# Kernel tuning notes

Hardware: AMD Instinct MI355X
Metric: run time of the kernel (lower is better)

## Reference

```python
import jax, jax.numpy as jnp
import numpy as np

B, S, E, H = 2, 2048, 1024, 16
HD = E // H  # head dim = 64
BASE = 10000.0


def _rope(x):
    # x: [b, h, s, hd]; interleaved RoPE (pairs (2i, 2i+1) rotated)
    s, hd = x.shape[-2], x.shape[-1]
    theta = 1.0 / (BASE ** (jnp.arange(0, hd, 2, dtype=jnp.float32) / hd))  # [hd/2]
    enc = jnp.arange(s, dtype=jnp.float32)[:, None] * theta[None, :]        # [s, hd/2]
    enc = jnp.repeat(enc, 2, axis=-1)                                        # [s, hd] interleaved
    cos, sin = jnp.cos(enc), jnp.sin(enc)
    # rotate_half: (x1, x2) -> (-x2, x1) on interleaved pairs
    xp = x.reshape(*x.shape[:-1], hd // 2, 2)
    rot = jnp.stack((-xp[..., 1], xp[..., 0]), axis=-1).reshape(x.shape)
    return x * cos + rot * sin


def reference(x, w1, w2):
    b, s, e = x.shape
    qkv = jnp.einsum('bse,fe->bsf', x, w1)                 # [b, s, 3e]
    qkv = qkv.reshape(b, s, 3, H, HD)                      # 'b s (n h e)'
    q, k, v = (jnp.transpose(qkv[:, :, i], (0, 2, 1, 3)) for i in range(3))  # [b,h,s,hd]
    q, k = _rope(q), _rope(k)
    scale = 1.0 / jnp.sqrt(jnp.asarray(HD, dtype=x.dtype))
    scores = jnp.einsum('bhqd,bhkd->bhqk', q, k) * scale   # [b,h,s,s]
    attn = jax.nn.softmax(scores, axis=-1)
    o = jnp.einsum('bhqk,bhkd->bhqd', attn, v)             # [b,h,s,hd]
    o = jnp.transpose(o, (0, 2, 1, 3)).reshape(b, s, e)    # 'b h s e -> b s (h e)'
    return jnp.einsum('bse,fe->bsf', o, w2)


def setup_inputs() -> dict:
    key = jax.random.key(0)
    k1, k2, k3 = jax.random.split(key, 3)
    x = jax.random.normal(k1, (B, S, E), dtype=jnp.float32)
    w1 = jax.random.normal(k2, (3 * E, E), dtype=jnp.float32) * (E ** -0.5)
    w2 = jax.random.normal(k3, (E, E), dtype=jnp.float32) * (E ** -0.5)
    return {"x": x, "w1": w1, "w2": w2}
```

## Files before the change

kernel.cpp:

```cpp
#include <hip/hip_runtime.h>
#include <math.h>

typedef unsigned short u16;
typedef unsigned int u32;
typedef float f32x4 __attribute__((ext_vector_type(4)));
typedef float f32x16 __attribute__((ext_vector_type(16)));
typedef u32 u32x4 __attribute__((ext_vector_type(4)));

static const size_t TAB_B  = 0;
static const size_t QBF_B  = 524288;
static const size_t KBF_B  = 8912896;
static const size_t VTB_B  = 17301504;
static const size_t W2H_B  = 25690112;
static const size_t XBF_B  = 29884416;
static const size_t W1BF_B = 38273024;
static const size_t O16_B  = 29884416;

#if __has_builtin(__builtin_amdgcn_exp2f)
#define EXP2(x) __builtin_amdgcn_exp2f(x)
#else
#define EXP2(x) __expf(0.69314718056f * (x))
#endif

__device__ __forceinline__ u16 f2bf(float f) {
  u32 u = __builtin_bit_cast(u32, f);
  u += 0x7fffu + ((u >> 16) & 1u);
  return (u16)(u >> 16);
}
__device__ __forceinline__ float bf2f(u16 h) {
  return __builtin_bit_cast(float, (u32)h << 16);
}
__device__ __forceinline__ u16 f2h(float f) {
  _Float16 h = (_Float16)f;
  return __builtin_bit_cast(u16, h);
}
__device__ __forceinline__ u32 cvtpk(float a, float b) {
  u32 r;
  asm("v_cvt_pk_bf16_f32 %0, %1, %2" : "=v"(r) : "v"(a), "v"(b));
  return r;
}
__device__ __forceinline__ void plswap(u32& a, u32& b) {
  asm volatile("v_permlane32_swap_b32 %0, %1" : "+v"(a), "+v"(b));
}
__device__ __forceinline__ void mfma16(f32x4& d, u32x4 a, u32x4 b) {
  asm volatile("v_mfma_f32_16x16x32_bf16 %0, %1, %2, %0"
               : "+v"(d)
               : "v"(a), "v"(b));
}
__device__ __forceinline__ void mfma16f(f32x4& d, u32x4 a, u32x4 b) {
  asm volatile("v_mfma_f32_16x16x32_f16 %0, %1, %2, %0"
               : "+v"(d)
               : "v"(a), "v"(b));
}
__device__ __forceinline__ void mfma32(f32x16& d, u32x4 a, u32x4 b) {
  asm volatile("v_mfma_f32_32x32x16_bf16 %0, %1, %2, %0"
               : "+v"(d)
               : "v"(a), "v"(b));
}
__device__ __forceinline__ void gld16(const void* g, void* l) {
  __builtin_amdgcn_global_load_lds(
      (const __attribute__((address_space(1))) void*)(void*)g,
      (__attribute__((address_space(3))) void*)l, 16, 0, 0);
}
#define HZ()                                            \
  do {                                                  \
    asm volatile("s_nop 7\ns_nop 7\ns_nop 7\ns_nop 7"); \
    __builtin_amdgcn_sched_barrier(0);                  \
  } while (0)
#define BAR()                          \
  do {                                 \
    __builtin_amdgcn_s_barrier();      \
    __builtin_amdgcn_sched_barrier(0); \
  } while (0)

__global__ __launch_bounds__(256) void prep_kernel(
    const float* __restrict__ x, const float* __restrict__ w1,
    const float* __restrict__ w2, float2* __restrict__ tab,
    u16* __restrict__ xbf, u16* __restrict__ w1bf, u16* __restrict__ w2h) {
  const int blk = blockIdx.x;
  const int t = threadIdx.x;
  if (blk < 256) {
    const int idx = (blk << 8) + t;
    const int s = idx >> 5, i = idx & 31;
    double theta = pow(10000.0, -((double)(2 * i)) / 64.0);
    float ang = (float)s * (float)theta;
    tab[idx] = make_float2(cosf(ang), sinf(ang));
  } else if (blk < 1280) {
    int i = ((blk - 256) << 8) + t;
#pragma unroll
    for (int r = 0; r < 4; ++r, i += 262144) {
      float4 v = ((const float4*)x)[i];
      ushort4 o;
      o.x = f2bf(v.x); o.y = f2bf(v.y); o.z = f2bf(v.z); o.w = f2bf(v.w);
      ((ushort4*)xbf)[i] = o;
    }
  } else if (blk < 2048) {
    int i = ((blk - 1280) << 8) + t;
#pragma unroll
    for (int r = 0; r < 4; ++r, i += 196608) {
      float4 v = ((const float4*)w1)[i];
      ushort4 o;
      o.x = f2bf(v.x); o.y = f2bf(v.y); o.z = f2bf(v.z); o.w = f2bf(v.w);
      ((ushort4*)w1bf)[i] = o;
    }
  } else {
    int i = ((blk - 2048) << 8) + t;
#pragma unroll
    for (int r = 0; r < 4; ++r, i += 65536) {
      float4 v = ((const float4*)w2)[i];
      ushort4 o;
      o.x = f2h(v.x); o.y = f2h(v.y); o.z = f2h(v.z); o.w = f2h(v.w);
      ((ushort4*)w2h)[i] = o;
    }
  }
}

template <int MODE, int NI>
__global__ __launch_bounds__(256) void gemm_bt(
    const u16* __restrict__ Ahi, const u16* __restrict__ Bhi, int nbn, int nkb,
    int cpx, const float2* __restrict__ tab, u16* __restrict__ qd,
    u16* __restrict__ kd, u16* __restrict__ vtd, float* __restrict__ fout) {
  __shared__ __align__(16) char SMEM[MODE == 0 ? 34816 : 16384 + NI * 4096];
  char* As = SMEM;
  char* Bs = SMEM + 16384;
  const int bid = blockIdx.x;
  const int wgid = (bid & 7) * cpx + (bid >> 3);
  const int bm = wgid / nbn;
  const int bn = wgid % nbn;
  const int m0 = bm << 7;
  const int n0 = bn * (NI << 5);
  const int t = threadIdx.x;
  const int w = t >> 6;
  const int lane = t & 63;
  const int lr = lane & 15;
  const int lg = lane >> 4;
  const int wr0 = (w >> 1) << 6;
  const int wc0 = (w & 1) * (NI << 4);
  const int srow0 = t >> 3;
  const int sblk = t & 7;

  f32x4 acc[4][NI];
#pragma unroll
  for (int mi = 0; mi < 4; ++mi)
#pragma unroll
    for (int ni = 0; ni < NI; ++ni) acc[mi][ni] = (f32x4)0.0f;

  for (int kb = 0; kb < nkb; ++kb) {
    const int k0 = kb << 6;
    if (kb) __syncthreads();
#pragma unroll
    for (int r = 0; r < 4; ++r) {
      const int row = srow0 + (r << 5);
      const int g = sblk ^ (row & 7);
      gld16(Ahi + (size_t)(m0 + row) * 1024 + k0 + (g << 3),
            As + (r << 12) + (w << 10));
    }
#pragma unroll
    for (int r = 0; r < NI; ++r) {
      const int row = srow0 + (r << 5);
      const int g = sblk ^ (row & 7);
      gld16(Bhi + (size_t)(n0 + row) * 1024 + k0 + (g << 3),
            Bs + (r << 12) + (w << 10));
    }
    asm volatile("s_waitcnt vmcnt(0)" ::: "memory");
    __syncthreads();
#pragma unroll
    for (int kk = 0; kk < 2; ++kk) {
      u32x4 af[4], bf[NI];
#pragma unroll
      for (int mi = 0; mi < 4; ++mi) {
        const int row = wr0 + (mi << 4) + lr;
        af[mi] = *(const u32x4*)(As + row * 128 +
                                 ((((kk << 2) + lg) ^ (row & 7)) << 4));
      }
#pragma unroll
      for (int ni = 0; ni < NI; ++ni) {
        const int row = wc0 + (ni << 4) + lr;
        bf[ni] = *(const u32x4*)(Bs + row * 128 +
                                 ((((kk << 2) + lg) ^ (row & 7)) << 4));
      }
      asm volatile("s_nop 1");
      __builtin_amdgcn_s_setprio(1);
#pragma unroll
      for (int mi = 0; mi < 4; ++mi)
#pragma unroll
        for (int ni = 0; ni < NI; ++ni) {
          if constexpr (MODE == 1)
            mfma16f(acc[mi][ni], af[mi], bf[ni]);
          else
            mfma16(acc[mi][ni], af[mi], bf[ni]);
        }
      __builtin_amdgcn_s_setprio(0);
    }
  }
  HZ();
  if constexpr (MODE == 0) {
    if (n0 >= 2048) {
      u16* Vt = (u16*)SMEM;
      __syncthreads();
#pragma unroll
      for (int mi = 0; mi < 4; ++mi)
#pragma unroll
        for (int ni = 0; ni < NI; ++ni)
#pragma unroll
          for (int i = 0; i < 4; ++i) {
            const int dl = wc0 + (ni << 4) + lr;
            const int sl = wr0 + (mi << 4) + (lg << 2) + i;
            Vt[dl * 136 + sl] = f2bf(acc[mi][ni][i]);
          }
      __syncthreads();
      const int row = t >> 1;
      const int half = t & 1;
      const int hh2 = (n0 - 2048 + row) >> 6;
      const int d2 = (n0 - 2048 + row) & 63;
      const int b2 = m0 >> 11;
      u16* dst = vtd + (((size_t)(b2 * 16 + hh2) * 64 + d2) * 2048) +
                 (m0 & 2047) + half * 64;
      const u16* src = Vt + row * 136 + half * 64;
#pragma unroll
      for (int c = 0; c < 8; ++c)
        *(u32x4*)(dst + (c << 3)) = *(const u32x4*)(src + (c << 3));
      return;
    }
  }
#pragma unroll
  for (int mi = 0; mi < 4; ++mi)
#pragma unroll
    for (int ni = 0; ni < NI; ++ni)
#pragma unroll
      for (int i = 0; i < 4; ++i) {
        float val = acc[mi][ni][i];
        const int grow = m0 + wr0 + (mi << 4) + (lg << 2) + i;
        const int col = n0 + wc0 + (ni << 4) + lr;
        if (MODE == 0) {
          const int b = grow >> 11, s = grow & 2047;
          const int which = col >> 10, hh = (col >> 6) & 15, d = col & 63;
          const size_t base = (size_t)((b << 4) + hh);
          float other = __shfl_xor(val, 1);
          float2 cs = tab[(s << 5) + (d >> 1)];
          float r = (d & 1) ? fmaf(val, cs.x, other * cs.y)
                            : fmaf(val, cs.x, -other * cs.y);
          if (which == 0) r *= 0.18033688011f;
          u16* dstp = which ? kd : qd;
          dstp[(base * 2048 + s) * 64 + d] = f2bf(r);
        } else {
          fout[(size_t)grow * 1024 + col] = val;
        }
      }
}

__global__ __launch_bounds__(256) void attn_mfma(
    const u16* __restrict__ q, const u16* __restrict__ k,
    const u16* __restrict__ vt, u16* __restrict__ o16) {
  __shared__ __align__(16) char Ks[2][8192];
  __shared__ __align__(16) char Vs[2][8192];
  const int bid = blockIdx.x;
  const int swz = (bid & 7) * 64 + (bid >> 3);
  const int qt = swz & 15;
  const int hh = (swz >> 4) & 15;
  const int b = swz >> 8;
  const int t = threadIdx.x;
  const int w = t >> 6;
  const int lane = t & 63;
  const int lq = lane & 31;
  const int h = lane >> 5;

  const size_t bh = (size_t)((b << 4) + hh);
  const u16* qb = q + (bh * 2048 + (size_t)(qt * 128 + w * 32)) * 64;
  const u16* kb = k + bh * 2048 * 64;
  const u16* vb = vt + bh * 64 * 2048;

  u32x4 qf[4];
#pragma unroll
  for (int dk = 0; dk < 4; ++dk)
    qf[dk] = *(const u32x4*)(qb + lq * 64 + dk * 16 + h * 8);

  auto issue = [&](int kt_, int buf_) {
    const u16* ksrc = kb + kt_ * 4096;
#pragma unroll
    for (int r = 0; r < 2; ++r) {
      const int row = (t >> 3) + (r << 5);
      const int g = (t & 7) ^ (row & 7);
      gld16(ksrc + row * 64 + (g << 3), &Ks[buf_][(r << 12) + (w << 10)]);
      gld16(vb + (size_t)row * 2048 + kt_ * 64 + (g << 3),
            &Vs[buf_][(r << 12) + (w << 10)]);
    }
  };

  f32x16 oacc0 = (f32x16)0.0f, oacc1 = (f32x16)0.0f;
  float lrow = 0.0f;

  issue(0, 0);
  for (int kt = 0; kt < 32; ++kt) {
    const int cur = kt & 1;
    if (kt < 31) {
      issue(kt + 1, cur ^ 1);
      asm volatile("s_waitcnt vmcnt(4)" ::: "memory");
    } else {
      asm volatile("s_waitcnt vmcnt(0)" ::: "memory");
    }
    BAR();
    const char* Kc = Ks[cur];
    const char* Vc = Vs[cur];
    f32x16 s0 = (f32x16)0.0f, s1 = (f32x16)0.0f;
    __builtin_amdgcn_s_setprio(1);
#pragma unroll
    for (int dk = 0; dk < 4; ++dk) {
      const int c = (dk << 1) + h;
      u32x4 kf0 = *(const u32x4*)(Kc + lq * 128 + ((c ^ (lq & 7)) << 4));
      u32x4 kf1 = *(const u32x4*)(Kc + (32 + lq) * 128 + ((c ^ (lq & 7)) << 4));
      mfma32(s0, kf0, qf[dk]);
      mfma32(s1, kf1, qf[dk]);
    }
    __builtin_amdgcn_s_setprio(0);
    HZ();
    float lsum = 0.0f;
#pragma unroll
    for (int i = 0; i < 16; ++i) {
      s0[i] = EXP2(s0[i]);
      lsum += s0[i];
    }
#pragma unroll
    for (int i = 0; i < 16; ++i) {
      s1[i] = EXP2(s1[i]);
      lsum += s1[i];
    }
    lrow += lsum;
    u32x4 pa0, pa1, pa2, pa3;
    {
      u32 w0 = cvtpk(s0[0], s0[1]), w1 = cvtpk(s0[2], s0[3]);
      u32 w2 = cvtpk(s0[4], s0[5]), w3 = cvtpk(s0[6], s0[7]);
      u32 w4 = cvtpk(s0[8], s0[9]), w5 = cvtpk(s0[10], s0[11]);
      u32 w6 = cvtpk(s0[12], s0[13]), w7 = cvtpk(s0[14], s0[15]);
      plswap(w0, w2);
      plswap(w1, w3);
      plswap(w4, w6);
      plswap(w5, w7);
      pa0[0] = w0; pa0[1] = w1; pa0[2] = w2; pa0[3] = w3;
      pa1[0] = w4; pa1[1] = w5; pa1[2] = w6; pa1[3] = w7;
      u32 y0 = cvtpk(s1[0], s1[1]), y1 = cvtpk(s1[2], s1[3]);
      u32 y2 = cvtpk(s1[4], s1[5]), y3 = cvtpk(s1[6], s1[7]);
      u32 y4 = cvtpk(s1[8], s1[9]), y5 = cvtpk(s1[10], s1[11]);
      u32 y6 = cvtpk(s1[12], s1[13]), y7 = cvtpk(s1[14], s1[15]);
      plswap(y0, y2);
      plswap(y1, y3);
      plswap(y4, y6);
      plswap(y5, y7);
      pa2[0] = y0; pa2[1] = y1; pa2[2] = y2; pa2[3] = y3;
      pa3[0] = y4; pa3[1] = y5; pa3[2] = y6; pa3[3] = y7;
    }
    asm volatile("s_nop 2");
    __builtin_amdgcn_s_setprio(1);
#define PVSTEP(kbk, paf)                                                      \
  {                                                                           \
    const int c = ((kbk) << 1) + h;                                           \
    u32x4 vf0 = *(const u32x4*)(Vc + lq * 128 + ((c ^ (lq & 7)) << 4));       \
    u32x4 vf1 =                                                               \
        *(const u32x4*)(Vc + (32 + lq) * 128 + ((c ^ (lq & 7)) << 4));        \
    mfma32(oacc0, paf, vf0);                                                  \
    mfma32(oacc1, paf, vf1);                                                  \
  }
    PVSTEP(0, pa0)
    PVSTEP(1, pa1)
    PVSTEP(2, pa2)
    PVSTEP(3, pa3)
#undef PVSTEP
    __builtin_amdgcn_s_setprio(0);
    BAR();
  }
  HZ();
  const float invl = 1.0f / (lrow + __shfl_xor(lrow, 32));
#pragma unroll
  for (int r = 0; r < 16; ++r) {
    const int qr = (r & 3) + 8 * (r >> 2) + 4 * h;
    const float fr = __shfl(invl, qr);
    const size_t srow = (size_t)(b * 2048 + (qt << 7) + (w << 5) + qr);
    const size_t base = srow * 1024 + (hh << 6) + lq;
    o16[base] = f2h(oacc0[r] * fr);
    o16[base + 32] = f2h(oacc1[r] * fr);
  }
}

extern "C" void kernel_launch(void* const* d_in, const int* in_sizes, int n_in,
                              void* d_out, int out_size, void* d_ws,
                              size_t ws_size, hipStream_t stream) {
  const float* x = (const float*)d_in[0];
  const float* w1 = (const float*)d_in[1];
  const float* w2 = (const float*)d_in[2];
  char* ws = (char*)d_ws;
  float2* tab = (float2*)(ws + TAB_B);
  u16* qbf = (u16*)(ws + QBF_B);
  u16* kbf = (u16*)(ws + KBF_B);
  u16* vtbf = (u16*)(ws + VTB_B);
  u16* w2h = (u16*)(ws + W2H_B);
  u16* xbf = (u16*)(ws + XBF_B);
  u16* w1bf = (u16*)(ws + W1BF_B);
  u16* o16 = (u16*)(ws + O16_B);
  float* out = (float*)d_out;

  prep_kernel<<<dim3(2304), dim3(256), 0, stream>>>(x, w1, w2, tab, xbf, w1bf,
                                                    w2h);
  gemm_bt<0, 4><<<dim3(32 * 24), dim3(256), 0, stream>>>(
      xbf, w1bf, 24, 16, 96, tab, qbf, kbf, vtbf, nullptr);
  attn_mfma<<<dim3(512), dim3(256), 0, stream>>>(qbf, kbf, vtbf, o16);
  gemm_bt<1, 2><<<dim3(32 * 16), dim3(256), 0, stream>>>(
      o16, w2h, 16, 16, 64, nullptr, nullptr, nullptr, nullptr, out);
}
```

Measured before the change: 106.1 us.

## Software-pipeline attention loop with triple-buffered LDS and overlapped QK/softmax-PV

Moves the K/V LDS staging from double to triple buffering and restructures the key-tile loop so the QK^T MFMAs for the next tile are issued alongside the exp/convert/PV work for the previous tile. The loop is manually unrolled by two with rotating score registers and buffer pointers, plus a prologue and epilogue. The aim is to hide softmax VALU latency behind matrix work and keep prefetches two tiles ahead. In exchange it uses more LDS (48KB per block), which can reduce occupancy, and holds more live registers for the two score sets.

```diff
diff --git a/kernel.cpp b/kernel.cpp
--- a/kernel.cpp
+++ b/kernel.cpp
@@ -252,8 +252,8 @@
 __global__ __launch_bounds__(256) void attn_mfma(
     const u16* __restrict__ q, const u16* __restrict__ k,
     const u16* __restrict__ vt, u16* __restrict__ o16) {
-  __shared__ __align__(16) char Ks[2][8192];
-  __shared__ __align__(16) char Vs[2][8192];
+  __shared__ __align__(16) char Ks0[8192], Ks1[8192], Ks2[8192];
+  __shared__ __align__(16) char Vs0[8192], Vs1[8192], Vs2[8192];
   const int bid = blockIdx.x;
   const int swz = (bid & 7) * 64 + (bid >> 3);
   const int qt = swz & 15;
@@ -275,99 +275,138 @@
   for (int dk = 0; dk < 4; ++dk)
     qf[dk] = *(const u32x4*)(qb + lq * 64 + dk * 16 + h * 8);
 
-  auto issue = [&](int kt_, int buf_) {
+  auto issue = [&](int kt_, char* kb_, char* vb_) {
     const u16* ksrc = kb + kt_ * 4096;
 #pragma unroll
     for (int r = 0; r < 2; ++r) {
       const int row = (t >> 3) + (r << 5);
       const int g = (t & 7) ^ (row & 7);
-      gld16(ksrc + row * 64 + (g << 3), &Ks[buf_][(r << 12) + (w << 10)]);
+      gld16(ksrc + row * 64 + (g << 3), kb_ + (r << 12) + (w << 10));
       gld16(vb + (size_t)row * 2048 + kt_ * 64 + (g << 3),
-            &Vs[buf_][(r << 12) + (w << 10)]);
+            vb_ + (r << 12) + (w << 10));
     }
   };
 
   f32x16 oacc0 = (f32x16)0.0f, oacc1 = (f32x16)0.0f;
   float lrow = 0.0f;
-
-  issue(0, 0);
-  for (int kt = 0; kt < 32; ++kt) {
-    const int cur = kt & 1;
-    if (kt < 31) {
-      issue(kt + 1, cur ^ 1);
-      asm volatile("s_waitcnt vmcnt(4)" ::: "memory");
-    } else {
-      asm volatile("s_waitcnt vmcnt(0)" ::: "memory");
-    }
-    BAR();
-    const char* Kc = Ks[cur];
-    const char* Vc = Vs[cur];
-    f32x16 s0 = (f32x16)0.0f, s1 = (f32x16)0.0f;
-    __builtin_amdgcn_s_setprio(1);
-#pragma unroll
-    for (int dk = 0; dk < 4; ++dk) {
-      const int c = (dk << 1) + h;
-      u32x4 kf0 = *(const u32x4*)(Kc + lq * 128 + ((c ^ (lq & 7)) << 4));
-      u32x4 kf1 = *(const u32x4*)(Kc + (32 + lq) * 128 + ((c ^ (lq & 7)) << 4));
-      mfma32(s0, kf0, qf[dk]);
-      mfma32(s1, kf1, qf[dk]);
-    }
-    __builtin_amdgcn_s_setprio(0);
-    HZ();
-    float lsum = 0.0f;
-#pragma unroll
-    for (int i = 0; i < 16; ++i) {
-      s0[i] = EXP2(s0[i]);
-      lsum += s0[i];
-    }
-#pragma unroll
-    for (int i = 0; i < 16; ++i) {
-      s1[i] = EXP2(s1[i]);
-      lsum += s1[i];
-    }
-    lrow += lsum;
-    u32x4 pa0, pa1, pa2, pa3;
-    {
-      u32 w0 = cvtpk(s0[0], s0[1]), w1 = cvtpk(s0[2], s0[3]);
-      u32 w2 = cvtpk(s0[4], s0[5]), w3 = cvtpk(s0[6], s0[7]);
-      u32 w4 = cvtpk(s0[8], s0[9]), w5 = cvtpk(s0[10], s0[11]);
-      u32 w6 = cvtpk(s0[12], s0[13]), w7 = cvtpk(s0[14], s0[15]);
-      plswap(w0, w2);
-      plswap(w1, w3);
-      plswap(w4, w6);
-      plswap(w5, w7);
-      pa0[0] = w0; pa0[1] = w1; pa0[2] = w2; pa0[3] = w3;
-      pa1[0] = w4; pa1[1] = w5; pa1[2] = w6; pa1[3] = w7;
-      u32 y0 = cvtpk(s1[0], s1[1]), y1 = cvtpk(s1[2], s1[3]);
-      u32 y2 = cvtpk(s1[4], s1[5]), y3 = cvtpk(s1[6], s1[7]);
-      u32 y4 = cvtpk(s1[8], s1[9]), y5 = cvtpk(s1[10], s1[11]);
-      u32 y6 = cvtpk(s1[12], s1[13]), y7 = cvtpk(s1[14], s1[15]);
-      plswap(y0, y2);
-      plswap(y1, y3);
-      plswap(y4, y6);
-      plswap(y5, y7);
-      pa2[0] = y0; pa2[1] = y1; pa2[2] = y2; pa2[3] = y3;
-      pa3[0] = y4; pa3[1] = y5; pa3[2] = y6; pa3[3] = y7;
-    }
-    asm volatile("s_nop 2");
-    __builtin_amdgcn_s_setprio(1);
-#define PVSTEP(kbk, paf)                                                      \
+  f32x16 sa0, sa1, sb0, sb1;
+  char *kA = Ks0, *kB = Ks1, *kC = Ks2;
+  char *vA = Vs0, *vB = Vs1, *vC = Vs2;
+
+#define QKSTEP(S0, S1, KCUR)                                                   \
   {                                                                           \
-    const int c = ((kbk) << 1) + h;                                           \
-    u32x4 vf0 = *(const u32x4*)(Vc + lq * 128 + ((c ^ (lq & 7)) << 4));       \
-    u32x4 vf1 =                                                               \
-        *(const u32x4*)(Vc + (32 + lq) * 128 + ((c ^ (lq & 7)) << 4));        \
-    mfma32(oacc0, paf, vf0);                                                  \
-    mfma32(oacc1, paf, vf1);                                                  \
-  }
-    PVSTEP(0, pa0)
-    PVSTEP(1, pa1)
-    PVSTEP(2, pa2)
-    PVSTEP(3, pa3)
-#undef PVSTEP
-    __builtin_amdgcn_s_setprio(0);
-    BAR();
-  }
+    S0 = (f32x16)0.0f;                                                        \
+    S1 = (f32x16)0.0f;                                                        \
+    __builtin_amdgcn_s_setprio(1);                                            \
+    _Pragma("unroll") for (int dk = 0; dk < 4; ++dk) {                        \
+      const int c = (dk << 1) + h;                                            \
+      u32x4 kf0 = *(const u32x4*)((KCUR) + lq * 128 + ((c ^ (lq & 7)) << 4)); \
+      u32x4 kf1 =                                                             \
+          *(const u32x4*)((KCUR) + (32 + lq) * 128 + ((c ^ (lq & 7)) << 4));  \
+      mfma32(S0, kf0, qf[dk]);                                                \
+      mfma32(S1, kf1, qf[dk]);                                                \
+    }                                                                         \
+    __builtin_amdgcn_s_setprio(0);                                            \
+  }
+
+#define SMPV(S0, S1, VCUR)                                                    \
+  {                                                                           \
+    float lsum = 0.0f;                                                        \
+    _Pragma("unroll") for (int i = 0; i < 16; ++i) {                          \
+      S0[i] = EXP2(S0[i]);                                                    \
+      lsum += S0[i];                                                          \
+    }                                                                         \
+    _Pragma("unroll") for (int i = 0; i < 16; ++i) {                          \
+      S1[i] = EXP2(S1[i]);                                                    \
+      lsum += S1[i];                                                          \
+    }                                                                         \
+    lrow += lsum;                                                             \
+    u32x4 pa0, pa1, pa2, pa3;                                                 \
+    {                                                                         \
+      u32 w0 = cvtpk(S0[0], S0[1]), w1 = cvtpk(S0[2], S0[3]);                 \
+      u32 w2 = cvtpk(S0[4], S0[5]), w3 = cvtpk(S0[6], S0[7]);                 \
+      u32 w4 = cvtpk(S0[8], S0[9]), w5 = cvtpk(S0[10], S0[11]);               \
+      u32 w6 = cvtpk(S0[12], S0[13]), w7 = cvtpk(S0[14], S0[15]);             \
+      plswap(w0, w2);                                                         \
+      plswap(w1, w3);                                                         \
+      plswap(w4, w6);                                                         \
+      plswap(w5, w7);                                                         \
+      pa0[0] = w0; pa0[1] = w1; pa0[2] = w2; pa0[3] = w3;                     \
+      pa1[0] = w4; pa1[1] = w5; pa1[2] = w6; pa1[3] = w7;                     \
+      u32 y0 = cvtpk(S1[0], S1[1]), y1 = cvtpk(S1[2], S1[3]);                 \
+      u32 y2 = cvtpk(S1[4], S1[5]), y3 = cvtpk(S1[6], S1[7]);                 \
+      u32 y4 = cvtpk(S1[8], S1[9]), y5 = cvtpk(S1[10], S1[11]);               \
+      u32 y6 = cvtpk(S1[12], S1[13]), y7 = cvtpk(S1[14], S1[15]);             \
+      plswap(y0, y2);                                                         \
+      plswap(y1, y3);                                                         \
+      plswap(y4, y6);                                                         \
+      plswap(y5, y7);                                                         \
+      pa2[0] = y0; pa2[1] = y1; pa2[2] = y2; pa2[3] = y3;                     \
+      pa3[0] = y4; pa3[1] = y5; pa3[2] = y6; pa3[3] = y7;                     \
+    }                                                                         \
+    asm volatile("s_nop 2");                   \
+    __builtin_amdgcn_s_setprio(1);                                            \
+    {                                                                         \
+      u32x4 vf0, vf1;                                                         \
+      vf0 = *(const u32x4*)((VCUR) + lq * 128 + (((0 + h) ^ (lq & 7)) << 4)); \
+      vf1 = *(const u32x4*)((VCUR) + (32 + lq) * 128 +                        \
+                            (((0 + h) ^ (lq & 7)) << 4));                     \
+      mfma32(oacc0, pa0, vf0);                                                \
+      mfma32(oacc1, pa0, vf1);                                                \
+      vf0 = *(const u32x4*)((VCUR) + lq * 128 + (((2 + h) ^ (lq & 7)) << 4)); \
+      vf1 = *(const u32x4*)((VCUR) + (32 + lq) * 128 +                        \
+                            (((2 + h) ^ (lq & 7)) << 4));                     \
+      mfma32(oacc0, pa1, vf0);                                                \
+      mfma32(oacc1, pa1, vf1);                                                \
+      vf0 = *(const u32x4*)((VCUR) + lq * 128 + (((4 + h) ^ (lq & 7)) << 4)); \
+      vf1 = *(const u32x4*)((VCUR) + (32 + lq) * 128 +                        \
+                            (((4 + h) ^ (lq & 7)) << 4));                     \
+      mfma32(oacc0, pa2, vf0);                                                \
+      mfma32(oacc1, pa2, vf1);                                                \
+      vf0 = *(const u32x4*)((VCUR) + lq * 128 + (((6 + h) ^ (lq & 7)) << 4)); \
+      vf1 = *(const u32x4*)((VCUR) + (32 + lq) * 128 +                        \
+                            (((6 + h) ^ (lq & 7)) << 4));                     \
+      mfma32(oacc0, pa3, vf0);                                                \
+      mfma32(oacc1, pa3, vf1);                                                \
+    }                                                                         \
+    __builtin_amdgcn_s_setprio(0);                                            \
+  }
+
+#define BODY(KT, SP0, SP1, SN0, SN1)                                          \
+  {                                                                           \
+    if ((KT) + 2 < 32) {                                                      \
+      issue((KT) + 2, kC, vC);                                                \
+      asm volatile("s_waitcnt vmcnt(4)" ::: "memory");                        \
+    } else {                                                                  \
+      asm volatile("s_waitcnt vmcnt(0)" ::: "memory");                        \
+    }                                                                         \
+    BAR();                                                                    \
+    QKSTEP(SN0, SN1, kB)                                                      \
+    SMPV(SP0, SP1, vA)                                                        \
+    BAR();                                                                    \
+    {                                                                         \
+      char* tk = kA; kA = kB; kB = kC; kC = tk;                               \
+      char* tv = vA; vA = vB; vB = vC; vC = tv;                               \
+    }                                                                         \
+  }
+
+  issue(0, kA, vA);
+  issue(1, kB, vB);
+  asm volatile("s_waitcnt vmcnt(4)" ::: "memory");
+  BAR();
+  QKSTEP(sa0, sa1, kA)
+  HZ();
+  for (int p = 0; p < 15; ++p) {
+    const int kt = p << 1;
+    BODY(kt, sa0, sa1, sb0, sb1)
+    BODY(kt + 1, sb0, sb1, sa0, sa1)
+  }
+  BODY(30, sa0, sa1, sb0, sb1)
+  HZ();
+  SMPV(sb0, sb1, vA)
+#undef BODY
+#undef SMPV
+#undef QKSTEP
   HZ();
   const float invl = 1.0f / (lrow + __shfl_xor(lrow, 32));
 #pragma unroll
```

Result: no change. 105.5 us (-0.6%).

## Double attention KV tile to 128 keys per iteration with wider V swizzle

Applied to the files above, without the earlier changes.

The attention loop now stages 128 keys per iteration instead of 64, which halves the iteration count and the number of barriers. K and V LDS buffers double in size, and the V tile is laid out with 16-chunk rows and a matching XOR swizzle. Each iteration computes four score tiles and runs exp/pack/PV in two halves, and the row-sum exp accumulation now uses a tree reduction. The cost is more LDS (64KB per block) and more registers, which may lower occupancy.

```diff
diff --git a/kernel.cpp b/kernel.cpp
--- a/kernel.cpp
+++ b/kernel.cpp
@@ -252,8 +252,8 @@
 __global__ __launch_bounds__(256) void attn_mfma(
     const u16* __restrict__ q, const u16* __restrict__ k,
     const u16* __restrict__ vt, u16* __restrict__ o16) {
-  __shared__ __align__(16) char Ks[2][8192];
-  __shared__ __align__(16) char Vs[2][8192];
+  __shared__ __align__(16) char Ks[2][16384];
+  __shared__ __align__(16) char Vs[2][16384];
   const int bid = blockIdx.x;
   const int swz = (bid & 7) * 64 + (bid >> 3);
   const int qt = swz & 15;
@@ -276,26 +276,85 @@
     qf[dk] = *(const u32x4*)(qb + lq * 64 + dk * 16 + h * 8);
 
   auto issue = [&](int kt_, int buf_) {
-    const u16* ksrc = kb + kt_ * 4096;
-#pragma unroll
-    for (int r = 0; r < 2; ++r) {
-      const int row = (t >> 3) + (r << 5);
-      const int g = (t & 7) ^ (row & 7);
-      gld16(ksrc + row * 64 + (g << 3), &Ks[buf_][(r << 12) + (w << 10)]);
-      gld16(vb + (size_t)row * 2048 + kt_ * 64 + (g << 3),
-            &Vs[buf_][(r << 12) + (w << 10)]);
+    const u16* ksrc = kb + (size_t)kt_ * 8192;
+#pragma unroll
+    for (int r = 0; r < 4; ++r) {
+      const int ci = (r << 8) + (w << 6) + lane;
+      const int dstb = ((r << 8) + (w << 6)) << 4;
+      {
+        const int row = ci >> 3, ch = ci & 7;
+        const int g = ch ^ (row & 7);
+        gld16(ksrc + row * 64 + (g << 3), &Ks[buf_][dstb]);
+      }
+      {
+        const int row = ci >> 4, ch = ci & 15;
+        const int g = ch ^ (row & 15);
+        gld16(vb + (size_t)row * 2048 + kt_ * 128 + (g << 3), &Vs[buf_][dstb]);
+      }
     }
   };
 
   f32x16 oacc0 = (f32x16)0.0f, oacc1 = (f32x16)0.0f;
   float lrow = 0.0f;
 
+#define EXPTREE(S)                                                            \
+  {                                                                           \
+    _Pragma("unroll") for (int i = 0; i < 16; ++i) S[i] = EXP2(S[i]);         \
+    float a0 = (S[0] + S[1]) + (S[2] + S[3]);                                 \
+    float a1 = (S[4] + S[5]) + (S[6] + S[7]);                                 \
+    float a2 = (S[8] + S[9]) + (S[10] + S[11]);                               \
+    float a3 = (S[12] + S[13]) + (S[14] + S[15]);                             \
+    lrow += (a0 + a1) + (a2 + a3);                                            \
+  }
+
+#define PACK(S0, S1)                                                          \
+  {                                                                           \
+    u32 w0 = cvtpk(S0[0], S0[1]), w1 = cvtpk(S0[2], S0[3]);                   \
+    u32 w2 = cvtpk(S0[4], S0[5]), w3 = cvtpk(S0[6], S0[7]);                   \
+    u32 w4 = cvtpk(S0[8], S0[9]), w5 = cvtpk(S0[10], S0[11]);                 \
+    u32 w6 = cvtpk(S0[12], S0[13]), w7 = cvtpk(S0[14], S0[15]);               \
+    plswap(w0, w2);                                                           \
+    plswap(w1, w3);                                                           \
+    plswap(w4, w6);                                                           \
+    plswap(w5, w7);                                                           \
+    pa0[0] = w0; pa0[1] = w1; pa0[2] = w2; pa0[3] = w3;                       \
+    pa1[0] = w4; pa1[1] = w5; pa1[2] = w6; pa1[3] = w7;                       \
+    u32 y0 = cvtpk(S1[0], S1[1]), y1 = cvtpk(S1[2], S1[3]);                   \
+    u32 y2 = cvtpk(S1[4], S1[5]), y3 = cvtpk(S1[6], S1[7]);                   \
+    u32 y4 = cvtpk(S1[8], S1[9]), y5 = cvtpk(S1[10], S1[11]);                 \
+    u32 y6 = cvtpk(S1[12], S1[13]), y7 = cvtpk(S1[14], S1[15]);               \
+    plswap(y0, y2);                                                           \
+    plswap(y1, y3);                                                           \
+    plswap(y4, y6);                                                           \
+    plswap(y5, y7);                                                           \
+    pa2[0] = y0; pa2[1] = y1; pa2[2] = y2; pa2[3] = y3;                       \
+    pa3[0] = y4; pa3[1] = y5; pa3[2] = y6; pa3[3] = y7;                       \
+  }
+
+#define PVH(VCUR, JB)                                                         \
+  asm volatile("s_nop 2");                                                    \
+  __builtin_amdgcn_s_setprio(1);                                              \
+  {                                                                           \
+    u32x4 vf0, vf1;                                                           \
+    _Pragma("unroll") for (int kbk = 0; kbk < 4; ++kbk) {                     \
+      const int jc = (JB) + (kbk << 1) + h;                                   \
+      const int co = (jc ^ (lq & 15)) << 4;                                   \
+      vf0 = *(const u32x4*)((VCUR) + lq * 256 + co);                          \
+      vf1 = *(const u32x4*)((VCUR) + (32 + lq) * 256 + co);                   \
+      if (kbk == 0) { mfma32(oacc0, pa0, vf0); mfma32(oacc1, pa0, vf1); }     \
+      if (kbk == 1) { mfma32(oacc0, pa1, vf0); mfma32(oacc1, pa1, vf1); }     \
+      if (kbk == 2) { mfma32(oacc0, pa2, vf0); mfma32(oacc1, pa2, vf1); }     \
+      if (kbk == 3) { mfma32(oacc0, pa3, vf0); mfma32(oacc1, pa3, vf1); }     \
+    }                                                                         \
+  }                                                                           \
+  __builtin_amdgcn_s_setprio(0);
+
   issue(0, 0);
-  for (int kt = 0; kt < 32; ++kt) {
+  for (int kt = 0; kt < 16; ++kt) {
     const int cur = kt & 1;
-    if (kt < 31) {
+    if (kt < 15) {
       issue(kt + 1, cur ^ 1);
-      asm volatile("s_waitcnt vmcnt(4)" ::: "memory");
+      asm volatile("s_waitcnt vmcnt(8)" ::: "memory");
     } else {
       asm volatile("s_waitcnt vmcnt(0)" ::: "memory");
     }
@@ -303,71 +362,41 @@
     const char* Kc = Ks[cur];
     const char* Vc = Vs[cur];
     f32x16 s0 = (f32x16)0.0f, s1 = (f32x16)0.0f;
+    f32x16 s2 = (f32x16)0.0f, s3 = (f32x16)0.0f;
     __builtin_amdgcn_s_setprio(1);
 #pragma unroll
     for (int dk = 0; dk < 4; ++dk) {
-      const int c = (dk << 1) + h;
-      u32x4 kf0 = *(const u32x4*)(Kc + lq * 128 + ((c ^ (lq & 7)) << 4));
-      u32x4 kf1 = *(const u32x4*)(Kc + (32 + lq) * 128 + ((c ^ (lq & 7)) << 4));
+      const int co = ((((dk << 1) + h) ^ (lq & 7)) << 4);
+      u32x4 kf0 = *(const u32x4*)(Kc + lq * 128 + co);
+      u32x4 kf1 = *(const u32x4*)(Kc + (32 + lq) * 128 + co);
+      u32x4 kf2 = *(const u32x4*)(Kc + (64 + lq) * 128 + co);
+      u32x4 kf3 = *(const u32x4*)(Kc + (96 + lq) * 128 + co);
       mfma32(s0, kf0, qf[dk]);
       mfma32(s1, kf1, qf[dk]);
+      mfma32(s2, kf2, qf[dk]);
+      mfma32(s3, kf3, qf[dk]);
     }
     __builtin_amdgcn_s_setprio(0);
     HZ();
-    float lsum = 0.0f;
-#pragma unroll
-    for (int i = 0; i < 16; ++i) {
-      s0[i] = EXP2(s0[i]);
-      lsum += s0[i];
-    }
-#pragma unroll
-    for (int i = 0; i < 16; ++i) {
-      s1[i] = EXP2(s1[i]);
-      lsum += s1[i];
-    }
-    lrow += lsum;
-    u32x4 pa0, pa1, pa2, pa3;
+    EXPTREE(s0)
+    EXPTREE(s1)
     {
-      u32 w0 = cvtpk(s0[0], s0[1]), w1 = cvtpk(s0[2], s0[3]);
-      u32 w2 = cvtpk(s0[4], s0[5]), w3 = cvtpk(s0[6], s0[7]);
-      u32 w4 = cvtpk(s0[8], s0[9]), w5 = cvtpk(s0[10], s0[11]);
-      u32 w6 = cvtpk(s0[12], s0[13]), w7 = cvtpk(s0[14], s0[15]);
-      plswap(w0, w2);
-      plswap(w1, w3);
-      plswap(w4, w6);
-      plswap(w5, w7);
-      pa0[0] = w0; pa0[1] = w1; pa0[2] = w2; pa0[3] = w3;
-      pa1[0] = w4; pa1[1] = w5; pa1[2] = w6; pa1[3] = w7;
-      u32 y0 = cvtpk(s1[0], s1[1]), y1 = cvtpk(s1[2], s1[3]);
-      u32 y2 = cvtpk(s1[4], s1[5]), y3 = cvtpk(s1[6], s1[7]);
-      u32 y4 = cvtpk(s1[8], s1[9]), y5 = cvtpk(s1[10], s1[11]);
-      u32 y6 = cvtpk(s1[12], s1[13]), y7 = cvtpk(s1[14], s1[15]);
-      plswap(y0, y2);
-      plswap(y1, y3);
-      plswap(y4, y6);
-      plswap(y5, y7);
-      pa2[0] = y0; pa2[1] = y1; pa2[2] = y2; pa2[3] = y3;
-      pa3[0] = y4; pa3[1] = y5; pa3[2] = y6; pa3[3] = y7;
-    }
-    asm volatile("s_nop 2");
-    __builtin_amdgcn_s_setprio(1);
-#define PVSTEP(kbk, paf)                                                      \
-  {                                                                           \
-    const int c = ((kbk) << 1) + h;                                           \
-    u32x4 vf0 = *(const u32x4*)(Vc + lq * 128 + ((c ^ (lq & 7)) << 4));       \
-    u32x4 vf1 =                                                               \
-        *(const u32x4*)(Vc + (32 + lq) * 128 + ((c ^ (lq & 7)) << 4));        \
-    mfma32(oacc0, paf, vf0);                                                  \
-    mfma32(oacc1, paf, vf1);                                                  \
-  }
-    PVSTEP(0, pa0)
-    PVSTEP(1, pa1)
-    PVSTEP(2, pa2)
-    PVSTEP(3, pa3)
-#undef PVSTEP
-    __builtin_amdgcn_s_setprio(0);
+      u32x4 pa0, pa1, pa2, pa3;
+      PACK(s0, s1)
+      PVH(Vc, 0)
+    }
+    EXPTREE(s2)
+    EXPTREE(s3)
+    {
+      u32x4 pa0, pa1, pa2, pa3;
+      PACK(s2, s3)
+      PVH(Vc, 8)
+    }
     BAR();
   }
+#undef PVH
+#undef PACK
+#undef EXPTREE
   HZ();
   const float invl = 1.0f / (lrow + __shfl_xor(lrow, 32));
 #pragma unroll
```

Result: no change. 105.9 us (-0.2%).
